# Optimization experiments

Hardware: AMD Instinct MI355X
Metric: run time of the kernel (lower is better)

The kernel has to match this reference:

```python
import jax, jax.numpy as jnp
import numpy as np

N = 20000   # nodes
E = 40000   # directed edges
F_IN = 13   # dataset.num_features
G = 1000    # graphs in batch
DIMS = [(13, 32), (32, 64), (64, 64)]  # (M_in, M_out) per NNConv layer


def setup_inputs() -> dict:
    key = jax.random.key(0)
    ks = list(jax.random.split(key, 32))
    inp = {}
    inp["x"] = jax.random.normal(ks[0], (N, F_IN), jnp.float32)
    inp["edge_index"] = jax.random.randint(ks[1], (2, E), 0, N, dtype=jnp.int32)
    inp["edge_attr"] = jax.random.uniform(ks[2], (E, 5), dtype=jnp.float32)
    inp["batch"] = jnp.sort(jax.random.randint(ks[3], (N,), 0, G, dtype=jnp.int32))
    i = 4
    for l, (mi, mo) in enumerate(DIMS):
        inp[f"w1_{l}"] = jax.random.normal(ks[i], (5, 128), jnp.float32) / np.sqrt(5.0).astype(np.float32); i += 1
        inp[f"b1_{l}"] = jnp.zeros((128,), jnp.float32)
        inp[f"w2_{l}"] = jax.random.normal(ks[i], (128, mi * mo), jnp.float32) / np.sqrt(128.0).astype(np.float32); i += 1
        inp[f"b2_{l}"] = jnp.zeros((mi * mo,), jnp.float32)
        inp[f"root_{l}"] = jax.random.normal(ks[i], (mi, mo), jnp.float32) / np.sqrt(float(mi)).astype(np.float32); i += 1
        inp[f"bias_{l}"] = jnp.zeros((mo,), jnp.float32)
    inp["fc1_w"] = jax.random.normal(ks[i], (64, 32), jnp.float32) / 8.0; i += 1
    inp["fc1_b"] = jnp.zeros((32,), jnp.float32)
    inp["fc2_w"] = jax.random.normal(ks[i], (32, 16), jnp.float32) / np.sqrt(32.0).astype(np.float32); i += 1
    inp["fc2_b"] = jnp.zeros((16,), jnp.float32)
    inp["fc3_w"] = jax.random.normal(ks[i], (16, 1), jnp.float32) / 4.0; i += 1
    inp["fc3_b"] = jnp.zeros((1,), jnp.float32)
    return inp


def _nnconv(x, src, dst, edge_attr, w1, b1, w2, b2, root, bias, mi, mo):
    # edge MLP: [E,5] -> [E,128] -> [E, mi*mo] per-edge weight matrices
    h = jax.nn.relu(edge_attr @ w1 + b1)
    We = (h @ w2 + b2).reshape(-1, mi, mo)          # [E, mi, mo]
    msg = jnp.einsum('ei,eio->eo', x[src], We)      # gather + per-edge matmul
    agg = jax.ops.segment_sum(msg, dst, num_segments=x.shape[0])  # scatter-add
    return x @ root + agg + bias                    # NNConv root weight + bias


def _forward(x, edge_index, edge_attr, batch, convs, fc1_w, fc1_b, fc2_w, fc2_b, fc3_w, fc3_b):
    src, dst = edge_index[0], edge_index[1]
    for (mi, mo), (w1, b1, w2, b2, root, bias) in zip(DIMS, convs):
        x = jax.nn.elu(_nnconv(x, src, dst, edge_attr, w1, b1, w2, b2, root, bias, mi, mo))
    # scatter_mean pooling over graphs
    sums = jax.ops.segment_sum(x, batch, num_segments=G)
    cnt = jax.ops.segment_sum(jnp.ones((x.shape[0],), x.dtype), batch, num_segments=G)
    xg = sums / jnp.maximum(cnt, 1.0)[:, None]
    xg = jax.nn.elu(xg @ fc1_w + fc1_b)
    xg = jax.nn.elu(xg @ fc2_w + fc2_b)
    return (xg @ fc3_w + fc3_b).reshape(-1)


def reference(x, edge_index, edge_attr, batch,
              w1_0, b1_0, w2_0, b2_0, root_0, bias_0,
              w1_1, b1_1, w2_1, b2_1, root_1, bias_1,
              w1_2, b1_2, w2_2, b2_2, root_2, bias_2,
              fc1_w, fc1_b, fc2_w, fc2_b, fc3_w, fc3_b):
    convs = [(w1_0, b1_0, w2_0, b2_0, root_0, bias_0),
             (w1_1, b1_1, w2_1, b2_1, root_1, bias_1),
             (w1_2, b1_2, w2_2, b2_2, root_2, bias_2)]
    return _forward(x, edge_index, edge_attr, batch, convs,
                    fc1_w, fc1_b, fc2_w, fc2_b, fc3_w, fc3_b)
```

## Files before the change

kernel.cpp:

```cpp
#include <hip/hip_runtime.h>
#include <stdint.h>
#include <math.h>

typedef _Float16 half8_t __attribute__((ext_vector_type(8)));
typedef float floatx4 __attribute__((ext_vector_type(4)));

#define NN 20000
#define NE 40000
#define NG 1000
#define NBLK 313
#define NSPLIT 4

__global__ __launch_bounds__(1024) void prep_csr_kernel(
    const float* __restrict__ x, _Float16* __restrict__ e16,
    const float* __restrict__ w2a, const float* __restrict__ b2a, _Float16* __restrict__ oa,
    const float* __restrict__ w2b, const float* __restrict__ b2b, _Float16* __restrict__ ob,
    const float* __restrict__ w2c, const float* __restrict__ b2c, _Float16* __restrict__ oc,
    const int* __restrict__ dst, int* __restrict__ row_ptr, int* __restrict__ cursor)
{
  __shared__ int sdeg[20480];
  __shared__ int wsum[16];

  if (blockIdx.x == 0) {
    constexpr int CH = 20;
    int t = threadIdx.x;
    int lane = t & 63, w = t >> 6;
    for (int i = t; i < 20480; i += 1024) sdeg[i] = 0;
    __syncthreads();
    for (int e = t; e < NE; e += 1024) atomicAdd(&sdeg[dst[e]], 1);
    __syncthreads();
    int base = t * CH;
    int local[CH];
#pragma unroll
    for (int i = 0; i < CH; ++i) local[i] = sdeg[base + i];
    int s = 0;
#pragma unroll
    for (int i = 0; i < CH; ++i) s += local[i];
    int sc = s;
#pragma unroll
    for (int d = 1; d < 64; d <<= 1) {
      int v = __shfl_up(sc, d, 64);
      if (lane >= d) sc += v;
    }
    if (lane == 63) wsum[w] = sc;
    __syncthreads();
    if (w == 0 && lane < 16) {
      int v = wsum[lane];
      int scc = v;
#pragma unroll
      for (int d = 1; d < 16; d <<= 1) {
        int u = __shfl_up(scc, d, 64);
        if (lane >= d) scc += u;
      }
      wsum[lane] = scc - v;
    }
    __syncthreads();
    int run = wsum[w] + (sc - s);
#pragma unroll
    for (int i = 0; i < CH; ++i) {
      int n = base + i;
      if (n < NN) { row_ptr[n] = run; cursor[n] = run; run += local[i]; }
      else if (n == NN) row_ptr[NN] = run;
    }
    return;
  }

  if (blockIdx.x <= 313) {
    int idx = (blockIdx.x - 1) * 1024 + threadIdx.x;
    if (idx >= NN * 16) return;
    int n = idx >> 4, i = idx & 15;
    e16[idx] = (i < 13) ? (_Float16)x[(size_t)n * 13 + i] : (_Float16)0.f;
    return;
  }

  const int TOT0 = 68 * 2 * 64, TOT1 = 132 * 4 * 64, TOT2 = 264 * 4 * 64;
  int idx = (blockIdx.x - 314) * 1024 + threadIdx.x;
  const float *w2, *b2; _Float16* op; int mi, mo, mpsh, CT;
  if (idx < TOT0) { w2 = w2a; b2 = b2a; op = oa; mi = 13; mo = 32; mpsh = 4; CT = 2; }
  else if (idx < TOT0 + TOT1) { idx -= TOT0; w2 = w2b; b2 = b2b; op = ob; mi = 32; mo = 64; mpsh = 5; CT = 4; }
  else if (idx < TOT0 + TOT1 + TOT2) { idx -= TOT0 + TOT1; w2 = w2c; b2 = b2c; op = oc; mi = 64; mo = 64; mpsh = 6; CT = 4; }
  else return;
  int l = idx & 63;
  int ct = (idx >> 6) % CT;
  int c = idx / (64 * CT);
  int q = l >> 4;
  int n = ct * 16 + (l & 15);
  int mask = (1 << mpsh) - 1;
  half8_t v;
#pragma unroll
  for (int j = 0; j < 8; ++j) {
    int r = c * 32 + q * 8 + j;
    int k = r >> mpsh, i = r & mask;
    float f = 0.f;
    if (i < mi) {
      if (k < 128) f = w2[(size_t)(k * mi + i) * mo + n];
      else if (k == 128) f = b2[(size_t)i * mo + n];
    }
    v[j] = (_Float16)f;
  }
  *(half8_t*)(op + (size_t)idx * 8) = v;
}

template <int MIP, int MO, int NCC, int KCNT, int FILLB>
__global__ __launch_bounds__(256, 4) void msg9_kernel(
    const float* __restrict__ ea, const float* __restrict__ w1,
    const float* __restrict__ b1, const _Float16* __restrict__ xe,
    const int* __restrict__ src,
    const _Float16* __restrict__ w2h, _Float16* __restrict__ msgp,
    const int* __restrict__ dst, int* __restrict__ cursor, int* __restrict__ eids)
{
  if constexpr (FILLB) {
    if (blockIdx.x >= NBLK * NSPLIT) {
      int e = (blockIdx.x - NBLK * NSPLIT) * 256 + threadIdx.x;
      if (e < NE) { int p = atomicAdd(&cursor[dst[e]], 1); eids[p] = e; }
      return;
    }
  }
  constexpr int EPB = 128;
  constexpr int CT = MO / 16;
  constexpr int CHB = CT * 1024;
  constexpr int XV = (MIP == 64) ? 2 : 1;
  constexpr int KH = (KCNT + 1) >> 1;

  __shared__ uint4 wsb[2][CHB / 16];
  __shared__ _Float16 h16[KCNT * EPB];
  __shared__ float w1s[5 * 128 + 128];

  const int t = threadIdx.x;
  const int wave = t >> 6, lane = t & 63;
  const int l15 = lane & 15, q = lane >> 4;
  const int split = blockIdx.x / NBLK;
  const int e0 = (blockIdx.x % NBLK) * EPB;
  const int c0 = NCC * split;
  const int kg0 = KCNT * split;

  const char* wgp = (const char*)w2h + (size_t)c0 * CHB;
  uint4 ra4, rb4; uint2 ra2, rb2;
  if constexpr (CT == 4) {
    ra4 = *(const uint4*)(wgp + t * 16);
    rb4 = *(const uint4*)(wgp + CHB + t * 16);
  } else {
    ra2 = *(const uint2*)(wgp + t * 8);
    rb2 = *(const uint2*)(wgp + CHB + t * 8);
  }

  const int wbase = wave * 32;
  half8_t xf[2][XV];
#pragma unroll
  for (int s = 0; s < 2; ++s) {
    int eg = e0 + wbase + s * 16 + l15; if (eg >= NE) eg = NE - 1;
    const _Float16* xr = xe + (size_t)src[eg] * MIP;
    int i0 = (MIP == 16) ? (q & 1) * 8 : q * 8;
    xf[s][0] = *(const half8_t*)(xr + i0);
    if constexpr (MIP == 64)
      xf[s][XV - 1] = *(const half8_t*)(xr + 32 + q * 8);
  }

  const int te = t & 127;
  float ear[5];
  {
    int eg = e0 + te; if (eg >= NE) eg = NE - 1;
#pragma unroll
    for (int j = 0; j < 5; ++j) ear[j] = ea[(size_t)eg * 5 + j];
  }
  for (int i = t; i < 768; i += 256) w1s[i] = (i < 640) ? w1[i] : b1[i - 640];
  __syncthreads();

  {
    int kh = t >> 7;
    int klo = kh * KH;
    int khi = klo + KH; if (khi > KCNT) khi = KCNT;
    for (int kl = klo; kl < khi; ++kl) {
      int kg = kg0 + kl;
      float v;
      if (kg < 128) {
        v = w1s[640 + kg];
#pragma unroll
        for (int j = 0; j < 5; ++j) v = fmaf(ear[j], w1s[j * 128 + kg], v);
        v = fmaxf(v, 0.f);
      } else v = (kg == 128) ? 1.f : 0.f;
      h16[kl * EPB + te] = (_Float16)v;
    }
  }
  __syncthreads();

  floatx4 acc[2][CT];
#pragma unroll
  for (int s = 0; s < 2; ++s)
#pragma unroll
    for (int b = 0; b < CT; ++b) acc[s][b] = (floatx4){0.f, 0.f, 0.f, 0.f};

#pragma unroll 2
  for (int cc = 0; cc < NCC; ++cc) {
    const bool odd = (cc & 1) != 0;
    if constexpr (CT == 4) wsb[cc & 1][t] = odd ? rb4 : ra4;
    else ((uint2*)wsb[cc & 1])[t] = odd ? rb2 : ra2;
    if (cc + 2 < NCC) {
      const char* np = wgp + (size_t)(cc + 2) * CHB;
      if constexpr (CT == 4) {
        if (odd) rb4 = *(const uint4*)(np + t * 16); else ra4 = *(const uint4*)(np + t * 16);
      } else {
        if (odd) rb2 = *(const uint2*)(np + t * 8); else ra2 = *(const uint2*)(np + t * 8);
      }
    }
    __syncthreads();
    const _Float16* wb = (const _Float16*)wsb[cc & 1];
    half8_t bf[CT];
#pragma unroll
    for (int b = 0; b < CT; ++b)
      bf[b] = *(const half8_t*)(wb + (b * 64 + lane) * 8);
    int kl;
    if constexpr (MIP == 64) kl = cc >> 1;
    else if constexpr (MIP == 32) kl = cc;
    else kl = 2 * cc + (q >> 1);
#pragma unroll
    for (int s = 0; s < 2; ++s) {
      _Float16 hv = h16[kl * EPB + wbase + s * 16 + l15];
      half8_t af;
      if constexpr (MIP == 64) af = xf[s][cc & 1] * hv;
      else af = xf[s][0] * hv;
#pragma unroll
      for (int b = 0; b < CT; ++b)
        acc[s][b] = __builtin_amdgcn_mfma_f32_16x16x32_f16(af, bf[b], acc[s][b], 0, 0, 0);
    }
  }

#pragma unroll
  for (int s = 0; s < 2; ++s) {
    int rowb = wbase + s * 16 + q * 4;
#pragma unroll
    for (int b = 0; b < CT; ++b) {
      int n = b * 16 + l15;
#pragma unroll
      for (int r = 0; r < 4; ++r) {
        int row = rowb + r;
        int e = e0 + row;
        if (e < NE) msgp[((size_t)e * NSPLIT + split) * MO + n] = (_Float16)acc[s][b][r];
      }
    }
  }
}

template <int MIP, int NCC, int KCNT>
__global__ __launch_bounds__(256, 4) void msg9p_kernel(
    const float* __restrict__ ea, const float* __restrict__ w1,
    const float* __restrict__ b1, const _Float16* __restrict__ xe,
    const int* __restrict__ src,
    const _Float16* __restrict__ w2h, _Float16* __restrict__ msgp)
{
  constexpr int EPB = 128;
  constexpr int MO = 64;
  constexpr int CT = 4;
  constexpr int CHB = 4096;
  constexpr int XV = (MIP == 64) ? 2 : 1;
  constexpr int KH = (KCNT + 1) >> 1;
  static_assert((NCC & 1) == 0, "NCC must be even for paired chunks");

  __shared__ uint4 wsb[2][2][CHB / 16];
  __shared__ _Float16 h16[KCNT * EPB];
  __shared__ float w1s[5 * 128 + 128];

  const int t = threadIdx.x;
  const int wave = t >> 6, lane = t & 63;
  const int l15 = lane & 15, q = lane >> 4;
  const int split = blockIdx.x / NBLK;
  const int e0 = (blockIdx.x % NBLK) * EPB;
  const int c0 = NCC * split;
  const int kg0 = KCNT * split;

  const char* wgp = (const char*)w2h + (size_t)c0 * CHB;
  uint4 pA0 = *(const uint4*)(wgp + 0 * CHB + t * 16);
  uint4 pA1 = *(const uint4*)(wgp + 1 * CHB + t * 16);
  uint4 pB0 = *(const uint4*)(wgp + 2 * CHB + t * 16);
  uint4 pB1 = *(const uint4*)(wgp + 3 * CHB + t * 16);

  const int wbase = wave * 32;
  half8_t xf[2][XV];
#pragma unroll
  for (int s = 0; s < 2; ++s) {
    int eg = e0 + wbase + s * 16 + l15; if (eg >= NE) eg = NE - 1;
    const _Float16* xr = xe + (size_t)src[eg] * MIP;
    xf[s][0] = *(const half8_t*)(xr + q * 8);
    if constexpr (MIP == 64)
      xf[s][XV - 1] = *(const half8_t*)(xr + 32 + q * 8);
  }

  const int te = t & 127;
  float ear[5];
  {
    int eg = e0 + te; if (eg >= NE) eg = NE - 1;
#pragma unroll
    for (int j = 0; j < 5; ++j) ear[j] = ea[(size_t)eg * 5 + j];
  }
  for (int i = t; i < 768; i += 256) w1s[i] = (i < 640) ? w1[i] : b1[i - 640];
  __syncthreads();

  {
    int kh = t >> 7;
    int klo = kh * KH;
    int khi = klo + KH; if (khi > KCNT) khi = KCNT;
    for (int kl = klo; kl < khi; ++kl) {
      int kg = kg0 + kl;
      float v;
      if (kg < 128) {
        v = w1s[640 + kg];
#pragma unroll
        for (int j = 0; j < 5; ++j) v = fmaf(ear[j], w1s[j * 128 + kg], v);
        v = fmaxf(v, 0.f);
      } else v = (kg == 128) ? 1.f : 0.f;
      h16[kl * EPB + te] = (_Float16)v;
    }
  }
  __syncthreads();

  floatx4 acc[2][CT];
#pragma unroll
  for (int s = 0; s < 2; ++s)
#pragma unroll
    for (int b = 0; b < CT; ++b) acc[s][b] = (floatx4){0.f, 0.f, 0.f, 0.f};

#pragma unroll 2
  for (int ci = 0; ci < NCC / 2; ++ci) {
    const bool odd = (ci & 1) != 0;
    wsb[ci & 1][0][t] = odd ? pB0 : pA0;
    wsb[ci & 1][1][t] = odd ? pB1 : pA1;
    if (2 * ci + 4 < NCC) {
      const char* np = wgp + (size_t)(2 * ci + 4) * CHB;
      if (odd) pB0 = *(const uint4*)(np + t * 16); else pA0 = *(const uint4*)(np + t * 16);
    }
    if (2 * ci + 5 < NCC) {
      const char* np = wgp + (size_t)(2 * ci + 5) * CHB;
      if (odd) pB1 = *(const uint4*)(np + t * 16); else pA1 = *(const uint4*)(np + t * 16);
    }
    __syncthreads();
#pragma unroll
    for (int u = 0; u < 2; ++u) {
      const int cc = 2 * ci + u;
      const _Float16* wbu = (const _Float16*)wsb[ci & 1][u];
      half8_t bf[CT];
#pragma unroll
      for (int b = 0; b < CT; ++b)
        bf[b] = *(const half8_t*)(wbu + (b * 64 + lane) * 8);
      int kl;
      if constexpr (MIP == 64) kl = cc >> 1;
      else kl = cc;
#pragma unroll
      for (int s = 0; s < 2; ++s) {
        _Float16 hv = h16[kl * EPB + wbase + s * 16 + l15];
        half8_t af;
        if constexpr (MIP == 64) af = xf[s][cc & 1] * hv;
        else af = xf[s][0] * hv;
#pragma unroll
        for (int b = 0; b < CT; ++b)
          acc[s][b] = __builtin_amdgcn_mfma_f32_16x16x32_f16(af, bf[b], acc[s][b], 0, 0, 0);
      }
    }
  }

#pragma unroll
  for (int s = 0; s < 2; ++s) {
    int rowb = wbase + s * 16 + q * 4;
#pragma unroll
    for (int b = 0; b < CT; ++b) {
      int n = b * 16 + l15;
#pragma unroll
      for (int r = 0; r < 4; ++r) {
        int row = rowb + r;
        int e = e0 + row;
        if (e < NE) msgp[((size_t)e * NSPLIT + split) * MO + n] = (_Float16)acc[s][b][r];
      }
    }
  }
}

template <int MIN_, int XST, int MO, int FINAL>
__global__ __launch_bounds__(256) void gather_kernel(
    const _Float16* __restrict__ e16in, const float* __restrict__ root,
    const float* __restrict__ bias, const int* __restrict__ row_ptr,
    const int* __restrict__ eids, const _Float16* __restrict__ msgp,
    _Float16* __restrict__ oute, float* __restrict__ outf)
{
  constexpr int NPB = 256 / MO;
  int n = blockIdx.x * NPB + threadIdx.x / MO;
  int o = threadIdx.x % MO;
  if (n >= NN) return;
  float a = bias[o];
#pragma unroll
  for (int i = 0; i < MIN_; ++i)
    a = fmaf((float)e16in[(size_t)n * XST + i], root[i * MO + o], a);
  int r0 = row_ptr[n], r1 = row_ptr[n + 1];
  float a2 = 0.f;
  int j = r0;
  for (; j + 1 < r1; j += 2) {
    int e1 = eids[j], e2 = eids[j + 1];
    const _Float16* p1 = msgp + (size_t)e1 * NSPLIT * MO + o;
    const _Float16* p2 = msgp + (size_t)e2 * NSPLIT * MO + o;
#pragma unroll
    for (int s = 0; s < NSPLIT; ++s) {
      a  += (float)p1[s * MO];
      a2 += (float)p2[s * MO];
    }
  }
  if (j < r1) {
    int e = eids[j];
    const _Float16* ep = msgp + (size_t)e * NSPLIT * MO + o;
#pragma unroll
    for (int s = 0; s < NSPLIT; ++s)
      a += (float)ep[s * MO];
  }
  a += a2;
  if constexpr (FINAL) {
    outf[(size_t)n * MO + o] = a;
  } else {
    float v = a > 0.f ? a : (expf(a) - 1.f);
    oute[(size_t)n * MO + o] = (_Float16)v;
  }
}

__global__ __launch_bounds__(256) void pool_fc_kernel(
    const float* __restrict__ xn2, const int* __restrict__ batch,
    const float* __restrict__ f1w, const float* __restrict__ f1b,
    const float* __restrict__ f2w, const float* __restrict__ f2b,
    const float* __restrict__ f3w, const float* __restrict__ f3b,
    float* __restrict__ out)
{
  __shared__ float xg4[4][64];
  __shared__ float xg[64]; __shared__ float a1[32]; __shared__ float a2[16];
  int g = blockIdx.x, t = threadIdx.x;
  int ch = t & 63, seg = t >> 6;
  int lo = 0, hi = NN;
  while (lo < hi) { int m = (lo + hi) >> 1; if (batch[m] < g) lo = m + 1; else hi = m; }
  int start = lo; hi = NN;
  while (lo < hi) { int m = (lo + hi) >> 1; if (batch[m] <= g) lo = m + 1; else hi = m; }
  int end = lo;
  float acc = 0.f;
  for (int n = start + seg; n < end; n += 4) {
    float v = xn2[(size_t)n * 64 + ch];
    acc += v > 0.f ? v : (expf(v) - 1.f);
  }
  xg4[seg][ch] = acc;
  __syncthreads();
  if (t < 64) {
    float c = (end > start) ? (float)(end - start) : 1.f;
    xg[t] = (xg4[0][t] + xg4[1][t] + xg4[2][t] + xg4[3][t]) / c;
  }
  __syncthreads();
  if (t < 32) {
    float a = f1b[t];
    for (int i = 0; i < 64; ++i) a = fmaf(xg[i], f1w[i * 32 + t], a);
    a1[t] = a > 0.f ? a : (expf(a) - 1.f);
  }
  __syncthreads();
  if (t < 16) {
    float a = f2b[t];
    for (int i = 0; i < 32; ++i) a = fmaf(a1[i], f2w[i * 16 + t], a);
    a2[t] = a > 0.f ? a : (expf(a) - 1.f);
  }
  __syncthreads();
  if (t == 0) {
    float a = f3b[0];
    for (int i = 0; i < 16; ++i) a = fmaf(a2[i], f3w[i], a);
    out[g] = a;
  }
}

extern "C" void kernel_launch(void* const* d_in, const int* in_sizes, int n_in,
                              void* d_out, int out_size, void* d_ws, size_t ws_size,
                              hipStream_t stream)
{
  const float* x_in  = (const float*)d_in[0];
  const int*   ei    = (const int*)d_in[1];
  const float* ea    = (const float*)d_in[2];
  const int*   batch = (const int*)d_in[3];
  const float* W1[3] = {(const float*)d_in[4],  (const float*)d_in[10], (const float*)d_in[16]};
  const float* B1[3] = {(const float*)d_in[5],  (const float*)d_in[11], (const float*)d_in[17]};
  const float* W2[3] = {(const float*)d_in[6],  (const float*)d_in[12], (const float*)d_in[18]};
  const float* B2[3] = {(const float*)d_in[7],  (const float*)d_in[13], (const float*)d_in[19]};
  const float* RT[3] = {(const float*)d_in[8],  (const float*)d_in[14], (const float*)d_in[20]};
  const float* BS[3] = {(const float*)d_in[9],  (const float*)d_in[15], (const float*)d_in[21]};
  const float* f1w = (const float*)d_in[22]; const float* f1b = (const float*)d_in[23];
  const float* f2w = (const float*)d_in[24]; const float* f2b = (const float*)d_in[25];
  const float* f3w = (const float*)d_in[26]; const float* f3b = (const float*)d_in[27];

  char* ws = (char*)d_ws;
  size_t off = 0;
  auto alloc = [&](size_t bytes) { void* p = ws + off; off += (bytes + 255) & ~(size_t)255; return p; };
  float*    xn2   = (float*)alloc((size_t)NN * 64 * 4);
  _Float16* e16_0 = (_Float16*)alloc((size_t)NN * 16 * 2);
  _Float16* e16_1 = (_Float16*)alloc((size_t)NN * 32 * 2);
  _Float16* e16_2 = (_Float16*)alloc((size_t)NN * 64 * 2);
  _Float16* w2h0  = (_Float16*)alloc((size_t)68 * 2048);
  _Float16* w2h1  = (_Float16*)alloc((size_t)132 * 4096);
  _Float16* w2h2  = (_Float16*)alloc((size_t)264 * 4096);
  _Float16* msgp  = (_Float16*)alloc((size_t)NSPLIT * NE * 64 * 2);
  int*      row_ptr = (int*)alloc((size_t)(NN + 1) * 4);
  int*      cursor  = (int*)alloc((size_t)NN * 4);
  int*      eids    = (int*)alloc((size_t)NE * 4);

  const int* srcp = ei;
  const int* dstp = ei + NE;

  prep_csr_kernel<<<422, 1024, 0, stream>>>(
      x_in, e16_0, W2[0], B2[0], w2h0, W2[1], B2[1], w2h1, W2[2], B2[2], w2h2,
      dstp, row_ptr, cursor);

  msg9_kernel<16, 32, 17, 34, 1><<<NBLK * NSPLIT + 157, 256, 0, stream>>>(
      ea, W1[0], B1[0], e16_0, srcp, w2h0, msgp, dstp, cursor, eids);
  gather_kernel<13, 16, 32, 0><<<(NN + 7) / 8, 256, 0, stream>>>(
      e16_0, RT[0], BS[0], row_ptr, eids, msgp, e16_1, xn2);

  msg9_kernel<32, 64, 33, 33, 0><<<NBLK * NSPLIT, 256, 0, stream>>>(
      ea, W1[1], B1[1], e16_1, srcp, w2h1, msgp, nullptr, nullptr, nullptr);
  gather_kernel<32, 32, 64, 0><<<(NN + 3) / 4, 256, 0, stream>>>(
      e16_1, RT[1], BS[1], row_ptr, eids, msgp, e16_2, xn2);

  msg9p_kernel<64, 66, 33><<<NBLK * NSPLIT, 256, 0, stream>>>(
      ea, W1[2], B1[2], e16_2, srcp, w2h2, msgp);
  gather_kernel<64, 64, 64, 1><<<(NN + 3) / 4, 256, 0, stream>>>(
      e16_2, RT[2], BS[2], row_ptr, eids, msgp, e16_2, xn2);

  pool_fc_kernel<<<NG, 256, 0, stream>>>(xn2, batch, f1w, f1b, f2w, f2b, f3w, f3b, (float*)d_out);
}
```

Measured before the change: 266.5 us.

## Process edges in destination-sorted order so gather reads contiguous messages

The message kernels now walk edges in CSR (destination-sorted) slot order through eids and write each message at its slot index. The gather kernels can then read contiguous message rows directly without the eids indirection. The eids fill moves out of the first message kernel into the single-block CSR prep block, which now does the cursor scatter in shared memory. This adds an indirection to the edge_attr and src loads and serialises more work in one block of the prep kernel.

```diff
diff --git a/kernel.cpp b/kernel.cpp
--- a/kernel.cpp
+++ b/kernel.cpp
@@ -16,7 +16,7 @@
     const float* __restrict__ w2a, const float* __restrict__ b2a, _Float16* __restrict__ oa,
     const float* __restrict__ w2b, const float* __restrict__ b2b, _Float16* __restrict__ ob,
     const float* __restrict__ w2c, const float* __restrict__ b2c, _Float16* __restrict__ oc,
-    const int* __restrict__ dst, int* __restrict__ row_ptr, int* __restrict__ cursor)
+    const int* __restrict__ dst, int* __restrict__ row_ptr, int* __restrict__ eids)
 {
   __shared__ int sdeg[20480];
   __shared__ int wsum[16];
@@ -59,8 +59,13 @@
 #pragma unroll
     for (int i = 0; i < CH; ++i) {
       int n = base + i;
-      if (n < NN) { row_ptr[n] = run; cursor[n] = run; run += local[i]; }
+      if (n < NN) { row_ptr[n] = run; sdeg[n] = run; run += local[i]; }
       else if (n == NN) row_ptr[NN] = run;
+    }
+    __syncthreads();
+    for (int e = t; e < NE; e += 1024) {
+      int p = atomicAdd(&sdeg[dst[e]], 1);
+      eids[p] = e;
     }
     return;
   }
@@ -101,21 +106,13 @@
   *(half8_t*)(op + (size_t)idx * 8) = v;
 }
 
-template <int MIP, int MO, int NCC, int KCNT, int FILLB>
+template <int MIP, int MO, int NCC, int KCNT>
 __global__ __launch_bounds__(256, 4) void msg9_kernel(
     const float* __restrict__ ea, const float* __restrict__ w1,
     const float* __restrict__ b1, const _Float16* __restrict__ xe,
-    const int* __restrict__ src,
-    const _Float16* __restrict__ w2h, _Float16* __restrict__ msgp,
-    const int* __restrict__ dst, int* __restrict__ cursor, int* __restrict__ eids)
+    const int* __restrict__ src, const int* __restrict__ eids,
+    const _Float16* __restrict__ w2h, _Float16* __restrict__ msgp)
 {
-  if constexpr (FILLB) {
-    if (blockIdx.x >= NBLK * NSPLIT) {
-      int e = (blockIdx.x - NBLK * NSPLIT) * 256 + threadIdx.x;
-      if (e < NE) { int p = atomicAdd(&cursor[dst[e]], 1); eids[p] = e; }
-      return;
-    }
-  }
   constexpr int EPB = 128;
   constexpr int CT = MO / 16;
   constexpr int CHB = CT * 1024;
@@ -148,8 +145,9 @@
   half8_t xf[2][XV];
 #pragma unroll
   for (int s = 0; s < 2; ++s) {
-    int eg = e0 + wbase + s * 16 + l15; if (eg >= NE) eg = NE - 1;
-    const _Float16* xr = xe + (size_t)src[eg] * MIP;
+    int sl = e0 + wbase + s * 16 + l15; if (sl >= NE) sl = NE - 1;
+    int ed = eids[sl];
+    const _Float16* xr = xe + (size_t)src[ed] * MIP;
     int i0 = (MIP == 16) ? (q & 1) * 8 : q * 8;
     xf[s][0] = *(const half8_t*)(xr + i0);
     if constexpr (MIP == 64)
@@ -159,9 +157,10 @@
   const int te = t & 127;
   float ear[5];
   {
-    int eg = e0 + te; if (eg >= NE) eg = NE - 1;
-#pragma unroll
-    for (int j = 0; j < 5; ++j) ear[j] = ea[(size_t)eg * 5 + j];
+    int sl = e0 + te; if (sl >= NE) sl = NE - 1;
+    int ed = eids[sl];
+#pragma unroll
+    for (int j = 0; j < 5; ++j) ear[j] = ea[(size_t)ed * 5 + j];
   }
   for (int i = t; i < 768; i += 256) w1s[i] = (i < 640) ? w1[i] : b1[i - 640];
   __syncthreads();
@@ -233,9 +232,8 @@
       int n = b * 16 + l15;
 #pragma unroll
       for (int r = 0; r < 4; ++r) {
-        int row = rowb + r;
-        int e = e0 + row;
-        if (e < NE) msgp[((size_t)e * NSPLIT + split) * MO + n] = (_Float16)acc[s][b][r];
+        int sl = e0 + rowb + r;
+        if (sl < NE) msgp[((size_t)sl * NSPLIT + split) * MO + n] = (_Float16)acc[s][b][r];
       }
     }
   }
@@ -245,7 +243,7 @@
 __global__ __launch_bounds__(256, 4) void msg9p_kernel(
     const float* __restrict__ ea, const float* __restrict__ w1,
     const float* __restrict__ b1, const _Float16* __restrict__ xe,
-    const int* __restrict__ src,
+    const int* __restrict__ src, const int* __restrict__ eids,
     const _Float16* __restrict__ w2h, _Float16* __restrict__ msgp)
 {
   constexpr int EPB = 128;
@@ -278,8 +276,9 @@
   half8_t xf[2][XV];
 #pragma unroll
   for (int s = 0; s < 2; ++s) {
-    int eg = e0 + wbase + s * 16 + l15; if (eg >= NE) eg = NE - 1;
-    const _Float16* xr = xe + (size_t)src[eg] * MIP;
+    int sl = e0 + wbase + s * 16 + l15; if (sl >= NE) sl = NE - 1;
+    int ed = eids[sl];
+    const _Float16* xr = xe + (size_t)src[ed] * MIP;
     xf[s][0] = *(const half8_t*)(xr + q * 8);
     if constexpr (MIP == 64)
       xf[s][XV - 1] = *(const half8_t*)(xr + 32 + q * 8);
@@ -288,9 +287,10 @@
   const int te = t & 127;
   float ear[5];
   {
-    int eg = e0 + te; if (eg >= NE) eg = NE - 1;
-#pragma unroll
-    for (int j = 0; j < 5; ++j) ear[j] = ea[(size_t)eg * 5 + j];
+    int sl = e0 + te; if (sl >= NE) sl = NE - 1;
+    int ed = eids[sl];
+#pragma unroll
+    for (int j = 0; j < 5; ++j) ear[j] = ea[(size_t)ed * 5 + j];
   }
   for (int i = t; i < 768; i += 256) w1s[i] = (i < 640) ? w1[i] : b1[i - 640];
   __syncthreads();
@@ -365,9 +365,8 @@
       int n = b * 16 + l15;
 #pragma unroll
       for (int r = 0; r < 4; ++r) {
-        int row = rowb + r;
-        int e = e0 + row;
-        if (e < NE) msgp[((size_t)e * NSPLIT + split) * MO + n] = (_Float16)acc[s][b][r];
+        int sl = e0 + rowb + r;
+        if (sl < NE) msgp[((size_t)sl * NSPLIT + split) * MO + n] = (_Float16)acc[s][b][r];
       }
     }
   }
@@ -377,7 +376,7 @@
 __global__ __launch_bounds__(256) void gather_kernel(
     const _Float16* __restrict__ e16in, const float* __restrict__ root,
     const float* __restrict__ bias, const int* __restrict__ row_ptr,
-    const int* __restrict__ eids, const _Float16* __restrict__ msgp,
+    const _Float16* __restrict__ msgp,
     _Float16* __restrict__ oute, float* __restrict__ outf)
 {
   constexpr int NPB = 256 / MO;
@@ -392,9 +391,8 @@
   float a2 = 0.f;
   int j = r0;
   for (; j + 1 < r1; j += 2) {
-    int e1 = eids[j], e2 = eids[j + 1];
-    const _Float16* p1 = msgp + (size_t)e1 * NSPLIT * MO + o;
-    const _Float16* p2 = msgp + (size_t)e2 * NSPLIT * MO + o;
+    const _Float16* p1 = msgp + (size_t)j * NSPLIT * MO + o;
+    const _Float16* p2 = msgp + (size_t)(j + 1) * NSPLIT * MO + o;
 #pragma unroll
     for (int s = 0; s < NSPLIT; ++s) {
       a  += (float)p1[s * MO];
@@ -402,8 +400,7 @@
     }
   }
   if (j < r1) {
-    int e = eids[j];
-    const _Float16* ep = msgp + (size_t)e * NSPLIT * MO + o;
+    const _Float16* ep = msgp + (size_t)j * NSPLIT * MO + o;
 #pragma unroll
     for (int s = 0; s < NSPLIT; ++s)
       a += (float)ep[s * MO];
@@ -494,7 +491,6 @@
   _Float16* w2h2  = (_Float16*)alloc((size_t)264 * 4096);
   _Float16* msgp  = (_Float16*)alloc((size_t)NSPLIT * NE * 64 * 2);
   int*      row_ptr = (int*)alloc((size_t)(NN + 1) * 4);
-  int*      cursor  = (int*)alloc((size_t)NN * 4);
   int*      eids    = (int*)alloc((size_t)NE * 4);
 
   const int* srcp = ei;
@@ -502,22 +498,22 @@
 
   prep_csr_kernel<<<422, 1024, 0, stream>>>(
       x_in, e16_0, W2[0], B2[0], w2h0, W2[1], B2[1], w2h1, W2[2], B2[2], w2h2,
-      dstp, row_ptr, cursor);
-
-  msg9_kernel<16, 32, 17, 34, 1><<<NBLK * NSPLIT + 157, 256, 0, stream>>>(
-      ea, W1[0], B1[0], e16_0, srcp, w2h0, msgp, dstp, cursor, eids);
+      dstp, row_ptr, eids);
+
+  msg9_kernel<16, 32, 17, 34><<<NBLK * NSPLIT, 256, 0, stream>>>(
+      ea, W1[0], B1[0], e16_0, srcp, eids, w2h0, msgp);
   gather_kernel<13, 16, 32, 0><<<(NN + 7) / 8, 256, 0, stream>>>(
-      e16_0, RT[0], BS[0], row_ptr, eids, msgp, e16_1, xn2);
-
-  msg9_kernel<32, 64, 33, 33, 0><<<NBLK * NSPLIT, 256, 0, stream>>>(
-      ea, W1[1], B1[1], e16_1, srcp, w2h1, msgp, nullptr, nullptr, nullptr);
+      e16_0, RT[0], BS[0], row_ptr, msgp, e16_1, xn2);
+
+  msg9_kernel<32, 64, 33, 33><<<NBLK * NSPLIT, 256, 0, stream>>>(
+      ea, W1[1], B1[1], e16_1, srcp, eids, w2h1, msgp);
   gather_kernel<32, 32, 64, 0><<<(NN + 3) / 4, 256, 0, stream>>>(
-      e16_1, RT[1], BS[1], row_ptr, eids, msgp, e16_2, xn2);
+      e16_1, RT[1], BS[1], row_ptr, msgp, e16_2, xn2);
 
   msg9p_kernel<64, 66, 33><<<NBLK * NSPLIT, 256, 0, stream>>>(
-      ea, W1[2], B1[2], e16_2, srcp, w2h2, msgp);
+      ea, W1[2], B1[2], e16_2, srcp, eids, w2h2, msgp);
   gather_kernel<64, 64, 64, 1><<<(NN + 3) / 4, 256, 0, stream>>>(
-      e16_2, RT[2], BS[2], row_ptr, eids, msgp, e16_2, xn2);
+      e16_2, RT[2], BS[2], row_ptr, msgp, e16_2, xn2);
 
   pool_fc_kernel<<<NG, 256, 0, stream>>>(xn2, batch, f1w, f1b, f2w, f2b, f3w, f3b, (float*)d_out);
 }
```

Measured after the change: 279.4 us. +4.8%, slower.
